# Optimization experiments

Hardware: AMD Instinct MI355X
Metric: run time of the kernel (lower is better)

## Reference

```python
import jax, jax.numpy as jnp
import numpy as np

H, DK = 8, 64  # n_head, d_k = n_feat // n_head
SCALE = 1.0 / np.sqrt(DK)


def setup_inputs() -> dict:
    key0 = jax.random.key(0)
    ks = jax.random.split(key0, 13)
    B, N, T1, T2, F = 16, 4, 256, 1024, 512
    query = jax.random.normal(ks[0], (B, T1, F), jnp.float32)
    key = jax.random.normal(ks[1], (B, N, T2, F), jnp.float32)
    value = jax.random.normal(ks[2], (B, N, T2, F), jnp.float32)
    mask_audio = jax.random.randint(ks[3], (B, N, 1, T2), 0, 2).astype(jnp.int32)
    # guarantee each candidate row has at least one valid key frame
    mask_audio = mask_audio.at[..., 0].set(1)
    mask_spk = jax.random.randint(ks[4], (B, N), 0, 2).astype(jnp.int32)
    # guarantee at least one valid candidate per batch item (avoids all -inf softmax)
    mask_spk = mask_spk.at[:, 0].set(1)
    s = 1.0 / np.sqrt(F)
    Wq = jax.random.normal(ks[5], (F, F), jnp.float32) * s
    bq = jax.random.normal(ks[6], (F,), jnp.float32) * 0.01
    Wk = jax.random.normal(ks[7], (F, F), jnp.float32) * s
    bk = jax.random.normal(ks[8], (F,), jnp.float32) * 0.01
    Wv = jax.random.normal(ks[9], (F, F), jnp.float32) * s
    bv = jax.random.normal(ks[10], (F,), jnp.float32) * 0.01
    Wo = jax.random.normal(ks[11], (F, F), jnp.float32) * s
    bo = jax.random.normal(ks[12], (F,), jnp.float32) * 0.01
    return dict(query=query, key=key, value=value, mask_audio=mask_audio,
                mask_spk=mask_spk, Wq=Wq, bq=bq, Wk=Wk, bk=bk, Wv=Wv, bv=bv,
                Wo=Wo, bo=bo)


def reference(query, key, value, mask_audio, mask_spk, Wq, bq, Wk, bk, Wv, bv, Wo, bo):
    B, T1, F = query.shape
    N, T2 = key.shape[1], key.shape[2]
    # projections (torch Linear: x @ W.T + b)
    q = (query @ Wq.T + bq).reshape(B, T1, H, DK)                 # (B,T1,H,DK)
    k = (key @ Wk.T + bk).reshape(B, N, T2, H, DK)                # (B,N,T2,H,DK)
    v = (value @ Wv.T + bv).reshape(B, N, T2, H, DK)
    # stage 1: intra-candidate temporal attention
    scores = jnp.einsum('bthd,bnshd->bnhts', q, k) * SCALE        # (B,N,H,T1,T2)
    ma = (mask_audio != 0)[:, :, None, :, :]                      # (B,N,1,1,T2)
    scores = jnp.where(ma, scores, -jnp.inf)
    attn1 = jnp.where(ma, jax.nn.softmax(scores, axis=-1), 0.0)
    phone = jnp.einsum('bnhts,bnshd->bnhtd', attn1, v)            # (B,N,H,T1,DK)
    # stage 2: inter-candidate attention
    ss = jnp.einsum('bthd,bnhtd->bthn', q, phone) * SCALE         # (B,T1,H,N)
    ms = (mask_spk != 0)[:, None, None, :]                        # (B,1,1,N)
    ss = jnp.where(ms, ss, -jnp.inf)
    attn2 = jnp.where(ms, jax.nn.softmax(ss, axis=-1), 0.0)
    x = jnp.einsum('bthn,bnhtd->bthd', attn2, phone).reshape(B, T1, H * DK)
    return x @ Wo.T + bo
```

## Files before the change

kernel.cpp:

```cpp
#include <hip/hip_runtime.h>
#include <hip/hip_bf16.h>
#include <math.h>

typedef __attribute__((ext_vector_type(4))) float  f32x4;
typedef __attribute__((ext_vector_type(4))) int    i32x4;
typedef __attribute__((ext_vector_type(8))) __bf16 bf16x8;
typedef __attribute__((ext_vector_type(8))) unsigned short u16x8;
typedef __attribute__((ext_vector_type(4))) unsigned short u16x4;

#define DEV static __device__ __forceinline__

#if __has_builtin(__builtin_amdgcn_permlane32_swap) && __has_builtin(__builtin_amdgcn_permlane16_swap)
#define HAVE_PERMLANE 1
#else
#define HAVE_PERMLANE 0
#endif

namespace {

constexpr int kB = 16, kT1 = 256, kF = 512, kN = 4, kT2 = 1024, kH = 8;
constexpr float kSCALE = 0.125f;
constexpr float kLOG2E = 1.4426950408889634f;

DEV unsigned short f2bf(float f) {
  union { float f; unsigned u; } c; c.f = f;
  unsigned u = c.u + 0x7fffu + ((c.u >> 16) & 1u);
  return (unsigned short)(u >> 16);
}
DEV float bf2f(unsigned short h) {
  union { unsigned u; float f; } c; c.u = ((unsigned)h) << 16;
  return c.f;
}

DEV void async_copy16(const void* g, void* l) {
  __builtin_amdgcn_global_load_lds(
      (const __attribute__((address_space(1))) unsigned int*)g,
      (__attribute__((address_space(3))) unsigned int*)l, 16, 0, 0);
}

DEV bf16x8 cvt8(f32x4 lo, f32x4 hi) {
  bf16x8 r;
  r[0] = (__bf16)lo[0]; r[1] = (__bf16)lo[1]; r[2] = (__bf16)lo[2]; r[3] = (__bf16)lo[3];
  r[4] = (__bf16)hi[0]; r[5] = (__bf16)hi[1]; r[6] = (__bf16)hi[2]; r[7] = (__bf16)hi[3];
  return r;
}

__global__ __launch_bounds__(256) void convert_w(
    const float* __restrict__ w0, const float* __restrict__ w1,
    const float* __restrict__ w2, const float* __restrict__ w3,
    unsigned short* __restrict__ o0, unsigned short* __restrict__ o1,
    unsigned short* __restrict__ o2, unsigned short* __restrict__ o3) {
  const int r = blockIdx.x >> 8;
  const int l = ((blockIdx.x & 255) * 256 + threadIdx.x) * 4;
  const float* src = r == 0 ? w0 : r == 1 ? w1 : r == 2 ? w2 : w3;
  unsigned short* dst = r == 0 ? o0 : r == 1 ? o1 : r == 2 ? o2 : o3;
  const float4 v = *(const float4*)(src + l);
  u16x4 q; q[0] = f2bf(v.x); q[1] = f2bf(v.y); q[2] = f2bf(v.z); q[3] = f2bf(v.w);
  *(u16x4*)(dst + l) = q;
}

template<int MODE>
__global__ __launch_bounds__(512, 2) void gemm256(
    const float* __restrict__ A, const unsigned short* __restrict__ Wb,
    const float* __restrict__ bias, unsigned short* __restrict__ outv) {
  __shared__ __align__(16) unsigned short As[2][256 * 64];
  __shared__ __align__(16) unsigned short Ws[2][256 * 64];
  const int t = threadIdx.x, lane = t & 63, wave = t >> 6;
  const int rb = blockIdx.x >> 1, cb = blockIdx.x & 1;
  const int wr = wave >> 2, wc = wave & 3;
  const int lq = lane & 15, lg = lane >> 4;
  const int arg = t >> 4, as16 = t & 15;

  f32x4 acc[8][4];
#pragma unroll
  for (int i = 0; i < 8; ++i)
#pragma unroll
    for (int j = 0; j < 4; ++j) acc[i][j] = f32x4{0.f, 0.f, 0.f, 0.f};

  f32x4 areg[8];
  bf16x8 af[4][2], bf[4][2];

#define A_ISSUE(kt)                                                             \
  do {                                                                          \
    _Pragma("unroll")                                                           \
    for (int j_ = 0; j_ < 8; ++j_)                                              \
      areg[j_] = *(const f32x4*)(A + (size_t)(rb * 256 + j_ * 32 + arg) * kF +  \
                                 (kt) * 64 + as16 * 4);                         \
  } while (0)

#define A_WRITE(dst)                                                            \
  do {                                                                          \
    _Pragma("unroll")                                                           \
    for (int j_ = 0; j_ < 8; ++j_) {                                            \
      const int row_ = j_ * 32 + arg;                                           \
      const int off_ = row_ * 64 + (((as16 >> 1) ^ (row_ & 7)) << 3) + (as16 & 1) * 4; \
      u16x4 pk_;                                                                \
      pk_[0] = f2bf(areg[j_][0]); pk_[1] = f2bf(areg[j_][1]);                   \
      pk_[2] = f2bf(areg[j_][2]); pk_[3] = f2bf(areg[j_][3]);                   \
      *(u16x4*)&(dst)[off_] = pk_;                                              \
    }                                                                           \
  } while (0)

#define W_ISSUE(kt, dst)                                                        \
  do {                                                                          \
    _Pragma("unroll")                                                           \
    for (int j_ = 0; j_ < 4; ++j_) {                                            \
      const int sidx_ = t + j_ * 512;                                           \
      const int row_ = sidx_ >> 3, s_ = sidx_ & 7;                              \
      async_copy16(Wb + (size_t)(cb * 256 + row_) * kF + (kt) * 64 +            \
                       ((s_ ^ (row_ & 7)) << 3),                                \
                   (dst) + (size_t)(j_ * 512 + wave * 64) * 8);                 \
    }                                                                           \
  } while (0)

#define RD_BF(pw)                                                               \
  do {                                                                          \
    _Pragma("unroll")                                                           \
    for (int n_ = 0; n_ < 4; ++n_) {                                            \
      const int br_ = wc * 64 + n_ * 16 + lq, x7_ = br_ & 7;                    \
      bf[n_][0] = *(const bf16x8*)&(pw)[br_ * 64 + ((lg ^ x7_) << 3)];          \
      bf[n_][1] = *(const bf16x8*)&(pw)[br_ * 64 + (((4 + lg) ^ x7_) << 3)];    \
    }                                                                           \
  } while (0)

#define RD_AF(pa, mb)                                                           \
  do {                                                                          \
    _Pragma("unroll")                                                           \
    for (int m_ = 0; m_ < 4; ++m_) {                                            \
      const int ar_ = wr * 128 + ((mb) + m_) * 16 + lq, x7_ = ar_ & 7;          \
      af[m_][0] = *(const bf16x8*)&(pa)[ar_ * 64 + ((lg ^ x7_) << 3)];          \
      af[m_][1] = *(const bf16x8*)&(pa)[ar_ * 64 + (((4 + lg) ^ x7_) << 3)];    \
    }                                                                           \
  } while (0)

#define MM(mb)                                                                  \
  do {                                                                          \
    _Pragma("unroll")                                                           \
    for (int kk_ = 0; kk_ < 2; ++kk_)                                           \
      _Pragma("unroll")                                                         \
      for (int m_ = 0; m_ < 4; ++m_)                                            \
        _Pragma("unroll")                                                       \
        for (int n_ = 0; n_ < 4; ++n_)                                          \
          acc[(mb) + m_][n_] = __builtin_amdgcn_mfma_f32_16x16x32_bf16(         \
              af[m_][kk_], bf[n_][kk_], acc[(mb) + m_][n_], 0, 0, 0);           \
  } while (0)

#define VMW0 asm volatile("s_waitcnt vmcnt(0)" ::: "memory")
#define LKW  asm volatile("s_waitcnt lgkmcnt(0)" ::: "memory")
#define SB   __builtin_amdgcn_sched_barrier(0)
#define BAR  do { __builtin_amdgcn_s_barrier(); __builtin_amdgcn_sched_barrier(0); } while (0)

  A_ISSUE(0); W_ISSUE(0, Ws[0]);
  VMW0; SB;
  A_WRITE(As[0]);
  LKW; BAR;

  unsigned short *pa = As[0], *qa = As[1], *pw = Ws[0], *qw = Ws[1];
#pragma unroll 1
  for (int kt = 0; kt < 8; ++kt) {
    if (kt < 7) { A_ISSUE(kt + 1); W_ISSUE(kt + 1, qw); }
    RD_BF(pw); RD_AF(pa, 0);
    LKW; SB;
    __builtin_amdgcn_s_setprio(1); MM(0); __builtin_amdgcn_s_setprio(0); SB;
    RD_AF(pa, 4);
    LKW; SB;
    __builtin_amdgcn_s_setprio(1); MM(4); __builtin_amdgcn_s_setprio(0); SB;
    if (kt < 7) { VMW0; SB; A_WRITE(qa); }
    LKW; BAR;
    { unsigned short* x = pa; pa = qa; qa = x; }
    { unsigned short* x = pw; pw = qw; qw = x; }
  }

#undef A_ISSUE
#undef A_WRITE
#undef W_ISSUE
#undef RD_BF
#undef RD_AF
#undef MM
#undef VMW0
#undef LKW
#undef SB
#undef BAR

  float bs4[4];
#pragma unroll
  for (int n = 0; n < 4; ++n) bs4[n] = bias[cb * 256 + wc * 64 + n * 16 + lq];

#pragma unroll
  for (int m = 0; m < 8; ++m) {
    const int row0 = rb * 256 + wr * 128 + m * 16 + lg * 4;
    const int bn = row0 >> 10, t2 = row0 & 1023;
#pragma unroll
    for (int n = 0; n < 4; ++n) {
      const int col = cb * 256 + wc * 64 + n * 16 + lq;
      const int h = col >> 6, d = col & 63;
      if (MODE == 3) {
        u16x4 pv;
#pragma unroll
        for (int j = 0; j < 4; ++j) pv[j] = f2bf(acc[m][n][j] + bs4[n]);
        *(u16x4*)&outv[(((size_t)(bn * kH + h)) * 64 + d) * kT2 + t2] = pv;
      } else {
#pragma unroll
        for (int j = 0; j < 4; ++j)
          outv[(((size_t)(bn * kH + h)) * kT2 + t2 + j) * 64 + d] =
              f2bf(acc[m][n][j] + bs4[n]);
      }
    }
  }
}

template<int MODE>
__global__ __launch_bounds__(256, 2) void gemm_mixed(
    const float* __restrict__ A, const unsigned short* __restrict__ Wb,
    const float* __restrict__ bias, void* __restrict__ outv, int nrb) {
  __shared__ __align__(16) unsigned short As[2][128 * 64];
  __shared__ __align__(16) unsigned short Bs[3][128 * 64];
  const int t = threadIdx.x, lane = t & 63, wave = t >> 6;
  const int w = blockIdx.x;
  const int xcd = w & 7, s = w >> 3;
  const int rb = xcd * (nrb >> 3) + (s >> 2);
  const int cb = s & 3;
  const int wr = wave >> 1, wc = wave & 1;
  const int lq = lane & 15, lg = lane >> 4;

  const int arow = t >> 1, ah = (t & 1) * 4;
  const float* aptr = A + (size_t)(rb * 128 + arow) * kF + ah * 8;

  f32x4 acc[4][4];
#pragma unroll
  for (int i = 0; i < 4; ++i)
#pragma unroll
    for (int j = 0; j < 4; ++j) acc[i][j] = f32x4{0.f, 0.f, 0.f, 0.f};

  f32x4 arA[8], arB[8];
  bf16x8 af[4][2], bfr[4][2];

#define A_LOAD(kb, ar)                                                          \
  do {                                                                          \
    const f32x4* p_ = (const f32x4*)(aptr + (kb) * 64);                         \
    ar[0]=p_[0]; ar[1]=p_[1]; ar[2]=p_[2]; ar[3]=p_[3];                         \
    ar[4]=p_[4]; ar[5]=p_[5]; ar[6]=p_[6]; ar[7]=p_[7];                         \
  } while (0)

#define A_CVT(ar, dst)                                                          \
  do {                                                                          \
    _Pragma("unroll")                                                           \
    for (int j_ = 0; j_ < 4; ++j_)                                              \
      *(bf16x8*)&(dst)[arow * 64 + (((ah + j_) ^ (arow & 7)) << 3)] =           \
          cvt8(ar[2*j_], ar[2*j_+1]);                                           \
  } while (0)

#define W_STAGE(kb, dst)                                                        \
  do {                                                                          \
    _Pragma("unroll")                                                           \
    for (int i_ = 0; i_ < 4; ++i_) {                                            \
      const int sidx_ = t + i_ * 256;                                           \
      const int row_ = sidx_ >> 3;                                              \
      const int gseg_ = (sidx_ & 7) ^ (row_ & 7);                               \
      async_copy16(Wb + (size_t)(cb * 128 + row_) * kF + (kb) * 64 + gseg_ * 8, \
                   (dst) + (size_t)(i_ * 256 + wave * 64) * 8);                 \
    }                                                                           \
  } while (0)

#define FRAG(Ap, Wp)                                                            \
  do {                                                                          \
    _Pragma("unroll")                                                           \
    for (int m_ = 0; m_ < 4; ++m_) {                                            \
      const int ar_ = wr * 64 + m_ * 16 + lq, x7_ = ar_ & 7;                    \
      af[m_][0] = *(const bf16x8*)&(Ap)[ar_ * 64 + ((lg       ^ x7_) << 3)];    \
      af[m_][1] = *(const bf16x8*)&(Ap)[ar_ * 64 + (((lg + 4) ^ x7_) << 3)];    \
    }                                                                           \
    _Pragma("unroll")                                                           \
    for (int n_ = 0; n_ < 4; ++n_) {                                            \
      const int br_ = wc * 64 + n_ * 16 + lq, x7_ = br_ & 7;                    \
      bfr[n_][0] = *(const bf16x8*)&(Wp)[br_ * 64 + ((lg       ^ x7_) << 3)];   \
      bfr[n_][1] = *(const bf16x8*)&(Wp)[br_ * 64 + (((lg + 4) ^ x7_) << 3)];   \
    }                                                                           \
  } while (0)

#define MFMA8                                                                   \
  do {                                                                          \
    _Pragma("unroll")                                                           \
    for (int kk_ = 0; kk_ < 2; ++kk_)                                           \
      _Pragma("unroll")                                                         \
      for (int m_ = 0; m_ < 4; ++m_)                                            \
        _Pragma("unroll")                                                       \
        for (int n_ = 0; n_ < 4; ++n_)                                          \
          acc[m_][n_] = __builtin_amdgcn_mfma_f32_16x16x32_bf16(                \
              af[m_][kk_], bfr[n_][kk_], acc[m_][n_], 0, 0, 0);                 \
  } while (0)

#define VMW(n) asm volatile("s_waitcnt vmcnt(" #n ")" ::: "memory")
#define LKW    asm volatile("s_waitcnt lgkmcnt(0)" ::: "memory")
#define BAR    do { __builtin_amdgcn_s_barrier(); __builtin_amdgcn_sched_barrier(0); } while (0)

  A_LOAD(0, arA); A_LOAD(1, arB);
  W_STAGE(0, Bs[0]); W_STAGE(1, Bs[1]);
  VMW(16);
  A_CVT(arA, As[0]);
  LKW; BAR;
  A_LOAD(2, arA); W_STAGE(2, Bs[2]);
  FRAG(As[0], Bs[0]); MFMA8;
  VMW(12); A_CVT(arB, As[1]); LKW; BAR;
  A_LOAD(3, arB); W_STAGE(3, Bs[0]);
  FRAG(As[1], Bs[1]); MFMA8;
  VMW(12); A_CVT(arA, As[0]); LKW; BAR;
  A_LOAD(4, arA); W_STAGE(4, Bs[1]);
  FRAG(As[0], Bs[2]); MFMA8;
  VMW(12); A_CVT(arB, As[1]); LKW; BAR;
  A_LOAD(5, arB); W_STAGE(5, Bs[2]);
  FRAG(As[1], Bs[0]); MFMA8;
  VMW(12); A_CVT(arA, As[0]); LKW; BAR;
  A_LOAD(6, arA); W_STAGE(6, Bs[0]);
  FRAG(As[0], Bs[1]); MFMA8;
  VMW(12); A_CVT(arB, As[1]); LKW; BAR;
  A_LOAD(7, arB); W_STAGE(7, Bs[1]);
  FRAG(As[1], Bs[2]); MFMA8;
  VMW(12); A_CVT(arA, As[0]); LKW; BAR;
  FRAG(As[0], Bs[0]); MFMA8;
  VMW(0); A_CVT(arB, As[1]); LKW; BAR;
  FRAG(As[1], Bs[1]); MFMA8;

#undef A_LOAD
#undef A_CVT
#undef W_STAGE
#undef FRAG
#undef MFMA8
#undef VMW
#undef LKW
#undef BAR

  float bs[4];
#pragma unroll
  for (int n2 = 0; n2 < 4; ++n2) bs[n2] = bias[cb*128 + wc*64 + n2*16 + lq];

#pragma unroll
  for (int m = 0; m < 4; ++m) {
#pragma unroll
    for (int n2 = 0; n2 < 4; ++n2) {
      const int col = cb*128 + wc*64 + n2*16 + lq;
      const int row0 = rb*128 + wr*64 + m*16 + lg*4;
#pragma unroll
      for (int j = 0; j < 4; ++j) {
        const int row = row0 + j;
        const float v = acc[m][n2][j] + bs[n2];
        if (MODE == 2) {
          ((float*)outv)[(size_t)row * kF + col] = v;
        } else {
          const int h = col >> 6, d = col & 63;
          const int b = row >> 8, t1i = row & 255;
          ((unsigned short*)outv)[(((size_t)(b * kH + h)) * kT1 + t1i) * 64 + d] = f2bf(v);
        }
      }
    }
  }
}

__global__ __launch_bounds__(512, 4) void attn_kernel(
    const unsigned short* __restrict__ qh, const unsigned short* __restrict__ kh,
    const unsigned short* __restrict__ vt, const int* __restrict__ mask_audio,
    unsigned short* __restrict__ phone) {
  __shared__ __align__(16) unsigned short Ks[2][64 * 64];
  __shared__ __align__(16) unsigned short Vs[2][64 * 64];
  __shared__ float Mb[2][64];
  const int t = threadIdx.x;
  const int lane = t & 63, wave = t >> 6;
  const int lq = lane & 15, lg = lane >> 4;
  const int bid = blockIdx.x;
  const int h = bid & 7, n = (bid >> 3) & 3, b = bid >> 5;
  const size_t qbase  = ((size_t)(b * kH + h)) * kT1 * 64;
  const size_t kvbase = ((size_t)((b * kN + n) * kH + h)) * kT2 * 64;
  const int* mbase = mask_audio + (size_t)(b * kN + n) * kT2;

  const int srow = (wave << 3) + (lane >> 3);
  const int sseg = lane & 7;
  const int sgx = (sseg ^ (srow & 7)) << 3;

#define STAGE_KV(c, buf)                                                          \
  do {                                                                            \
    async_copy16(kh + kvbase + ((size_t)(((c) << 6) + srow) << 6) + sgx,          \
                 &Ks[buf][wave << 9]);                                            \
    async_copy16(vt + kvbase + ((size_t)srow << 10) + ((c) << 6) + sgx,           \
                 &Vs[buf][wave << 9]);                                            \
  } while (0)

  bf16x8 qf[2][2];
#pragma unroll
  for (int qt = 0; qt < 2; ++qt) {
    const unsigned short* qp = qh + qbase + ((size_t)((wave << 5) + (qt << 4) + lq) << 6);
    qf[qt][0] = *(const bf16x8*)(qp + (lg << 3));
    qf[qt][1] = *(const bf16x8*)(qp + 32 + (lg << 3));
  }

  STAGE_KV(0, 0);
  if (t < 64) Mb[0][t] = mbase[t] ? 0.f : -1e30f;
  asm volatile("s_waitcnt vmcnt(0) lgkmcnt(0)" ::: "memory");
  __builtin_amdgcn_s_barrier();
  __builtin_amdgcn_sched_barrier(0);

  f32x4 of[2][4];
  float m2[2], l1[2];
#pragma unroll
  for (int qt = 0; qt < 2; ++qt) {
    m2[qt] = -INFINITY; l1[qt] = 0.f;
#pragma unroll
    for (int fd = 0; fd < 4; ++fd) of[qt][fd] = f32x4{0.f, 0.f, 0.f, 0.f};
  }
  const float sc2 = kSCALE * kLOG2E;

  int cur = 0;
#pragma unroll 1
  for (int c = 0; c < 16; ++c) {
    const int nxt = cur ^ 1;
    if (c < 15) {
      STAGE_KV(c + 1, nxt);
      if (t < 64) Mb[nxt][t] = mbase[((c + 1) << 6) + t] ? 0.f : -1e30f;
    }
    const unsigned short* Kb = Ks[cur];
    const unsigned short* Vb = Vs[cur];
    const float* mrow = Mb[cur];

    bf16x8 kf[4][2];
#pragma unroll
    for (int kt = 0; kt < 4; ++kt) {
      const int kr = kt * 16 + lq, x7 = kr & 7;
      kf[kt][0] = *(const bf16x8*)&Kb[kr * 64 + ((lg       ^ x7) << 3)];
      kf[kt][1] = *(const bf16x8*)&Kb[kr * 64 + (((lg + 4) ^ x7) << 3)];
    }

#pragma unroll
    for (int qt = 0; qt < 2; ++qt) {
      f32x4 sT[4];
#pragma unroll
      for (int kt = 0; kt < 4; ++kt) {
        f32x4 sv = f32x4{0.f, 0.f, 0.f, 0.f};
        sv = __builtin_amdgcn_mfma_f32_16x16x32_bf16(kf[kt][0], qf[qt][0], sv, 0, 0, 0);
        sv = __builtin_amdgcn_mfma_f32_16x16x32_bf16(kf[kt][1], qf[qt][1], sv, 0, 0, 0);
        sT[kt] = sv;
      }
      float scv[16];
#pragma unroll
      for (int kt = 0; kt < 4; ++kt) {
        const f32x4 mk = *(const f32x4*)&mrow[kt * 16 + lg * 4];
#pragma unroll
        for (int j = 0; j < 4; ++j)
          scv[kt*4+j] = fmaf(sT[kt][j], sc2, mk[j]);
      }
      float rmax = scv[0];
#pragma unroll
      for (int i = 1; i < 16; ++i) rmax = fmaxf(rmax, scv[i]);
      rmax = fmaxf(rmax, __shfl_xor(rmax, 16));
      rmax = fmaxf(rmax, __shfl_xor(rmax, 32));
      const float mold = m2[qt];
      if (!__all(rmax <= mold + 8.f)) {
        const float mnew = fmaxf(mold, rmax);
        const float rs = exp2f(mold - mnew);
        m2[qt] = mnew;
        l1[qt] *= rs;
        const float s0 = __shfl(rs, lg*4 + 0);
        const float s1 = __shfl(rs, lg*4 + 1);
        const float s2 = __shfl(rs, lg*4 + 2);
        const float s3 = __shfl(rs, lg*4 + 3);
#pragma unroll
        for (int fd = 0; fd < 4; ++fd) {
          of[qt][fd][0] *= s0; of[qt][fd][1] *= s1;
          of[qt][fd][2] *= s2; of[qt][fd][3] *= s3;
        }
      }
      const float mloc = m2[qt];
      float pf[16]; float psum = 0.f;
#pragma unroll
      for (int i = 0; i < 16; ++i) { const float p = exp2f(scv[i] - mloc); pf[i] = p; psum += p; }
      psum += __shfl_xor(psum, 16);
      psum += __shfl_xor(psum, 32);
      l1[qt] += psum;
      unsigned pk[8];
#pragma unroll
      for (int kt = 0; kt < 4; ++kt) {
        pk[2*kt]   = (unsigned)f2bf(pf[4*kt+0]) | ((unsigned)f2bf(pf[4*kt+1]) << 16);
        pk[2*kt+1] = (unsigned)f2bf(pf[4*kt+2]) | ((unsigned)f2bf(pf[4*kt+3]) << 16);
      }
      unsigned am0[4], am1[4];
#if HAVE_PERMLANE
      {
        auto x0 = __builtin_amdgcn_permlane32_swap((int)pk[0], (int)pk[2], false, false);
        auto y0 = __builtin_amdgcn_permlane16_swap(x0[0], x0[1], false, false);
        am0[0] = (unsigned)y0[0]; am0[2] = (unsigned)y0[1];
        auto x1 = __builtin_amdgcn_permlane32_swap((int)pk[1], (int)pk[3], false, false);
        auto y1 = __builtin_amdgcn_permlane16_swap(x1[0], x1[1], false, false);
        am0[1] = (unsigned)y1[0]; am0[3] = (unsigned)y1[1];
        auto x2 = __builtin_amdgcn_permlane32_swap((int)pk[4], (int)pk[6], false, false);
        auto y2 = __builtin_amdgcn_permlane16_swap(x2[0], x2[1], false, false);
        am1[0] = (unsigned)y2[0]; am1[2] = (unsigned)y2[1];
        auto x3 = __builtin_amdgcn_permlane32_swap((int)pk[5], (int)pk[7], false, false);
        auto y3 = __builtin_amdgcn_permlane16_swap(x3[0], x3[1], false, false);
        am1[1] = (unsigned)y3[0]; am1[3] = (unsigned)y3[1];
      }
#else
      {
        const int srcbase = (2 * (lg & 1)) * 16 + lq;
#pragma unroll
        for (int u = 0; u < 4; ++u) {
          const int src = srcbase + (u >> 1) * 16;
          const unsigned va0 = __shfl(pk[(u & 1)],     src);
          const unsigned vb0 = __shfl(pk[2 + (u & 1)], src);
          am0[u] = (lg & 2) ? vb0 : va0;
          const unsigned va1 = __shfl(pk[4 + (u & 1)], src);
          const unsigned vb1 = __shfl(pk[6 + (u & 1)], src);
          am1[u] = (lg & 2) ? vb1 : va1;
        }
      }
#endif
      union { unsigned u[4]; bf16x8 v; } A0, A1;
#pragma unroll
      for (int u = 0; u < 4; ++u) { A0.u[u] = am0[u]; A1.u[u] = am1[u]; }
#pragma unroll
      for (int fd = 0; fd < 4; ++fd) {
        const int d = fd * 16 + lq, x7d = d & 7;
        const bf16x8 vB0 = *(const bf16x8*)&Vb[d * 64 + ((lg       ^ x7d) << 3)];
        const bf16x8 vB1 = *(const bf16x8*)&Vb[d * 64 + (((lg + 4) ^ x7d) << 3)];
        of[qt][fd] = __builtin_amdgcn_mfma_f32_16x16x32_bf16(A0.v, vB0, of[qt][fd], 0, 0, 0);
        of[qt][fd] = __builtin_amdgcn_mfma_f32_16x16x32_bf16(A1.v, vB1, of[qt][fd], 0, 0, 0);
      }
    }
    asm volatile("s_waitcnt vmcnt(0) lgkmcnt(0)" ::: "memory");
    __builtin_amdgcn_s_barrier();
    __builtin_amdgcn_sched_barrier(0);
    cur = nxt;
  }
#undef STAGE_KV

  const size_t phbase = ((size_t)((b * kN + n) * kH + h)) * kT1 * 64;
#pragma unroll
  for (int qt = 0; qt < 2; ++qt) {
    const float li0 = 1.f / __shfl(l1[qt], lg*4 + 0);
    const float li1 = 1.f / __shfl(l1[qt], lg*4 + 1);
    const float li2 = 1.f / __shfl(l1[qt], lg*4 + 2);
    const float li3 = 1.f / __shfl(l1[qt], lg*4 + 3);
#pragma unroll
    for (int fd = 0; fd < 4; ++fd) {
      const int d = fd * 16 + lq;
      const size_t rowb = phbase + (size_t)((wave << 5) + qt*16 + lg*4) * 64 + d;
      phone[rowb]       = f2bf(of[qt][fd][0] * li0);
      phone[rowb + 64]  = f2bf(of[qt][fd][1] * li1);
      phone[rowb + 128] = f2bf(of[qt][fd][2] * li2);
      phone[rowb + 192] = f2bf(of[qt][fd][3] * li3);
    }
  }
}

__global__ __launch_bounds__(256) void stage2_kernel(
    const unsigned short* __restrict__ qh, const unsigned short* __restrict__ phone,
    const int* __restrict__ mask_spk, float* __restrict__ x) {
  const int t = threadIdx.x, lane = t & 63, wave = t >> 6;
  const int wid = blockIdx.x * 4 + wave;
  const int h = wid & 7;
  const int bt = wid >> 3;
  const int t1i = bt & 255, b = bt >> 8;
  const int d = lane;
  const float q = bf2f(qh[(((size_t)(b * kH + h)) * kT1 + t1i) * 64 + d]);
  float ph[4], ss[4];
#pragma unroll
  for (int n = 0; n < 4; ++n) {
    ph[n] = bf2f(phone[(((size_t)((b * kN + n) * kH + h)) * kT1 + t1i) * 64 + d]);
    float sv = q * ph[n];
#pragma unroll
    for (int o = 1; o < 64; o <<= 1) sv += __shfl_xor(sv, o);
    ss[n] = sv * kSCALE;
  }
  int msk[4];
#pragma unroll
  for (int n = 0; n < 4; ++n) msk[n] = mask_spk[b * kN + n];
  float mx = -INFINITY;
#pragma unroll
  for (int n = 0; n < 4; ++n) if (msk[n]) mx = fmaxf(mx, ss[n]);
  float e[4], sum = 0.f;
#pragma unroll
  for (int n = 0; n < 4; ++n) { const float v = msk[n] ? __expf(ss[n] - mx) : 0.f; e[n] = v; sum += v; }
  float xo = 0.f;
#pragma unroll
  for (int n = 0; n < 4; ++n) xo += e[n] * ph[n];
  xo /= sum;
  x[((size_t)(b * kT1 + t1i)) * kF + h * 64 + d] = xo;
}

}

extern "C" void kernel_launch(void* const* d_in, const int* in_sizes, int n_in,
                              void* d_out, int out_size, void* d_ws, size_t ws_size,
                              hipStream_t stream) {
  (void)in_sizes; (void)n_in; (void)out_size; (void)ws_size;
  const float* query = (const float*)d_in[0];
  const float* key   = (const float*)d_in[1];
  const float* value = (const float*)d_in[2];
  const int* mask_audio = (const int*)d_in[3];
  const int* mask_spk   = (const int*)d_in[4];
  const float* Wq = (const float*)d_in[5];  const float* bq = (const float*)d_in[6];
  const float* Wk = (const float*)d_in[7];  const float* bk = (const float*)d_in[8];
  const float* Wv = (const float*)d_in[9];  const float* bv = (const float*)d_in[10];
  const float* Wo = (const float*)d_in[11]; const float* bo = (const float*)d_in[12];
  float* out = (float*)d_out;

  unsigned short* qws  = (unsigned short*)d_ws;
  unsigned short* kws  = qws  + (size_t)kB * kH * kT1 * 64;
  unsigned short* vws  = kws  + (size_t)kB * kN * kH * kT2 * 64;
  unsigned short* phws = vws  + (size_t)kB * kN * kH * kT2 * 64;
  float*          xws  = (float*)(phws + (size_t)kB * kN * kH * kT1 * 64);
  unsigned short* wqb  = (unsigned short*)(xws + (size_t)kB * kT1 * kF);
  unsigned short* wkb  = wqb + (size_t)kF * kF;
  unsigned short* wvb  = wkb + (size_t)kF * kF;
  unsigned short* wob  = wvb + (size_t)kF * kF;

  convert_w<<<1024, 256, 0, stream>>>(Wq, Wk, Wv, Wo, wqb, wkb, wvb, wob);
  gemm_mixed<0><<<kB * kT1 / 128 * 4, 256, 0, stream>>>(query, wqb, bq, qws, kB * kT1 / 128);
  gemm256<1><<<kB * kN * kT2 / 256 * 2, 512, 0, stream>>>(key,   wkb, bk, kws);
  gemm256<3><<<kB * kN * kT2 / 256 * 2, 512, 0, stream>>>(value, wvb, bv, vws);
  attn_kernel<<<kB * kN * kH, 512, 0, stream>>>(qws, kws, vws, mask_audio, phws);
  stage2_kernel<<<kB * kT1 * kH / 4, 256, 0, stream>>>(qws, phws, mask_spk, xws);
  gemm_mixed<2><<<kB * kT1 / 128 * 4, 256, 0, stream>>>(xws, wob, bo, out, kB * kT1 / 128);
}
```

Before: 290.9 us.

## Deepen attention K/V pipeline to four buffers and precompute the audio mask bias

The attention kernel now keeps four K/V LDS buffers and prefetches two chunks ahead, with one barrier per iteration whose vmcnt wait is relaxed so loads overlap more compute. The audio mask bias for all 1024 keys is precomputed into LDS once, which removes the per-chunk mask staging. The row max and sum now use tree reductions, and f2bf uses the native bf16 cast. LDS use doubles, which may lower occupancy, and the single barrier placed before use needs care against buffer reuse. An unused W_STAGE variant is added, but the GEMM still uses the original staging.

Result: faster. 280.0 us (-3.8%).

```diff
diff --git a/kernel.cpp b/kernel.cpp
--- a/kernel.cpp
+++ b/kernel.cpp
@@ -23,9 +23,7 @@
 constexpr float kLOG2E = 1.4426950408889634f;
 
 DEV unsigned short f2bf(float f) {
-  union { float f; unsigned u; } c; c.f = f;
-  unsigned u = c.u + 0x7fffu + ((c.u >> 16) & 1u);
-  return (unsigned short)(u >> 16);
+  union { __bf16 h; unsigned short u; } c; c.h = (__bf16)f; return c.u;
 }
 DEV float bf2f(unsigned short h) {
   union { unsigned u; float f; } c; c.u = ((unsigned)h) << 16;
@@ -253,6 +251,23 @@
 #define W_STAGE(kb, dst)                                                        \
   do {                                                                          \
     _Pragma("unroll")                                                           \
+    for (int i_ = 0; i_ < 2; ++i_) {                                            \
+      const int sidx_ = t + i_ * 256;                                           \
+      const int row_ = sidx_ >> 2;                                              \
+      const int gseg_ = 0;                                                      \
+      (void)gseg_;                                                              \
+      const int r8_ = sidx_ >> 3;                                               \
+      const int s8_ = sidx_ & 7;                                                \
+      async_copy16(Wb + (size_t)(cb * 128 + r8_) * kF + (kb) * 64 +             \
+                       ((s8_ ^ (r8_ & 7)) << 3),                                \
+                   (dst) + (size_t)(i_ * 256 + wave * 64) * 8);                 \
+      (void)row_;                                                               \
+    }                                                                           \
+  } while (0)
+
+#define W_STAGE2(kb, dst)                                                       \
+  do {                                                                          \
+    _Pragma("unroll")                                                           \
     for (int i_ = 0; i_ < 4; ++i_) {                                            \
       const int sidx_ = t + i_ * 256;                                           \
       const int row_ = sidx_ >> 3;                                              \
@@ -295,26 +310,26 @@
 #define BAR    do { __builtin_amdgcn_s_barrier(); __builtin_amdgcn_sched_barrier(0); } while (0)
 
   A_LOAD(0, arA); A_LOAD(1, arB);
-  W_STAGE(0, Bs[0]); W_STAGE(1, Bs[1]);
+  W_STAGE2(0, Bs[0]); W_STAGE2(1, Bs[1]);
   VMW(16);
   A_CVT(arA, As[0]);
   LKW; BAR;
-  A_LOAD(2, arA); W_STAGE(2, Bs[2]);
+  A_LOAD(2, arA); W_STAGE2(2, Bs[2]);
   FRAG(As[0], Bs[0]); MFMA8;
   VMW(12); A_CVT(arB, As[1]); LKW; BAR;
-  A_LOAD(3, arB); W_STAGE(3, Bs[0]);
+  A_LOAD(3, arB); W_STAGE2(3, Bs[0]);
   FRAG(As[1], Bs[1]); MFMA8;
   VMW(12); A_CVT(arA, As[0]); LKW; BAR;
-  A_LOAD(4, arA); W_STAGE(4, Bs[1]);
+  A_LOAD(4, arA); W_STAGE2(4, Bs[1]);
   FRAG(As[0], Bs[2]); MFMA8;
   VMW(12); A_CVT(arB, As[1]); LKW; BAR;
-  A_LOAD(5, arB); W_STAGE(5, Bs[2]);
+  A_LOAD(5, arB); W_STAGE2(5, Bs[2]);
   FRAG(As[1], Bs[0]); MFMA8;
   VMW(12); A_CVT(arA, As[0]); LKW; BAR;
-  A_LOAD(6, arA); W_STAGE(6, Bs[0]);
+  A_LOAD(6, arA); W_STAGE2(6, Bs[0]);
   FRAG(As[0], Bs[1]); MFMA8;
   VMW(12); A_CVT(arB, As[1]); LKW; BAR;
-  A_LOAD(7, arB); W_STAGE(7, Bs[1]);
+  A_LOAD(7, arB); W_STAGE2(7, Bs[1]);
   FRAG(As[1], Bs[2]); MFMA8;
   VMW(12); A_CVT(arA, As[0]); LKW; BAR;
   FRAG(As[0], Bs[0]); MFMA8;
@@ -324,6 +339,7 @@
 #undef A_LOAD
 #undef A_CVT
 #undef W_STAGE
+#undef W_STAGE2
 #undef FRAG
 #undef MFMA8
 #undef VMW
@@ -360,9 +376,9 @@
     const unsigned short* __restrict__ qh, const unsigned short* __restrict__ kh,
     const unsigned short* __restrict__ vt, const int* __restrict__ mask_audio,
     unsigned short* __restrict__ phone) {
-  __shared__ __align__(16) unsigned short Ks[2][64 * 64];
-  __shared__ __align__(16) unsigned short Vs[2][64 * 64];
-  __shared__ float Mb[2][64];
+  __shared__ __align__(16) unsigned short Ks[4][64 * 64];
+  __shared__ __align__(16) unsigned short Vs[4][64 * 64];
+  __shared__ float Mbias[1024];
   const int t = threadIdx.x;
   const int lane = t & 63, wave = t >> 6;
   const int lq = lane & 15, lg = lane >> 4;
@@ -384,6 +400,13 @@
                  &Vs[buf][wave << 9]);                                            \
   } while (0)
 
+  {
+    const int i0 = t * 2;
+    const int m0 = mbase[i0], m1 = mbase[i0 + 1];
+    Mbias[i0]     = m0 ? 0.f : -1e30f;
+    Mbias[i0 + 1] = m1 ? 0.f : -1e30f;
+  }
+
   bf16x8 qf[2][2];
 #pragma unroll
   for (int qt = 0; qt < 2; ++qt) {
@@ -393,10 +416,8 @@
   }
 
   STAGE_KV(0, 0);
-  if (t < 64) Mb[0][t] = mbase[t] ? 0.f : -1e30f;
-  asm volatile("s_waitcnt vmcnt(0) lgkmcnt(0)" ::: "memory");
-  __builtin_amdgcn_s_barrier();
-  __builtin_amdgcn_sched_barrier(0);
+  STAGE_KV(1, 1);
+  asm volatile("s_waitcnt lgkmcnt(0)" ::: "memory");
 
   f32x4 of[2][4];
   float m2[2], l1[2];
@@ -408,17 +429,18 @@
   }
   const float sc2 = kSCALE * kLOG2E;
 
-  int cur = 0;
 #pragma unroll 1
   for (int c = 0; c < 16; ++c) {
-    const int nxt = cur ^ 1;
-    if (c < 15) {
-      STAGE_KV(c + 1, nxt);
-      if (t < 64) Mb[nxt][t] = mbase[((c + 1) << 6) + t] ? 0.f : -1e30f;
-    }
-    const unsigned short* Kb = Ks[cur];
-    const unsigned short* Vb = Vs[cur];
-    const float* mrow = Mb[cur];
+    if (c < 14) STAGE_KV(c + 2, (c + 2) & 3);
+    if (c < 14)      asm volatile("s_waitcnt vmcnt(4)" ::: "memory");
+    else if (c == 14) asm volatile("s_waitcnt vmcnt(2)" ::: "memory");
+    else              asm volatile("s_waitcnt vmcnt(0)" ::: "memory");
+    __builtin_amdgcn_s_barrier();
+    __builtin_amdgcn_sched_barrier(0);
+
+    const unsigned short* Kb = Ks[c & 3];
+    const unsigned short* Vb = Vs[c & 3];
+    const float* mrow = Mbias + (c << 6);
 
     bf16x8 kf[4][2];
 #pragma unroll
@@ -446,9 +468,12 @@
         for (int j = 0; j < 4; ++j)
           scv[kt*4+j] = fmaf(sT[kt][j], sc2, mk[j]);
       }
-      float rmax = scv[0];
-#pragma unroll
-      for (int i = 1; i < 16; ++i) rmax = fmaxf(rmax, scv[i]);
+      const float x0 = fmaxf(fmaxf(scv[0],  scv[1]),  scv[2]);
+      const float x1 = fmaxf(fmaxf(scv[3],  scv[4]),  scv[5]);
+      const float x2 = fmaxf(fmaxf(scv[6],  scv[7]),  scv[8]);
+      const float x3 = fmaxf(fmaxf(scv[9],  scv[10]), scv[11]);
+      const float x4 = fmaxf(fmaxf(scv[12], scv[13]), scv[14]);
+      float rmax = fmaxf(fmaxf(fmaxf(x0, x1), x2), fmaxf(fmaxf(x3, x4), scv[15]));
       rmax = fmaxf(rmax, __shfl_xor(rmax, 16));
       rmax = fmaxf(rmax, __shfl_xor(rmax, 32));
       const float mold = m2[qt];
@@ -468,9 +493,14 @@
         }
       }
       const float mloc = m2[qt];
-      float pf[16]; float psum = 0.f;
-#pragma unroll
-      for (int i = 0; i < 16; ++i) { const float p = exp2f(scv[i] - mloc); pf[i] = p; psum += p; }
+      float pf[16];
+#pragma unroll
+      for (int i = 0; i < 16; ++i) pf[i] = exp2f(scv[i] - mloc);
+      const float a0 = (pf[0] + pf[1]) + (pf[2] + pf[3]);
+      const float a1 = (pf[4] + pf[5]) + (pf[6] + pf[7]);
+      const float a2 = (pf[8] + pf[9]) + (pf[10] + pf[11]);
+      const float a3 = (pf[12] + pf[13]) + (pf[14] + pf[15]);
+      float psum = (a0 + a1) + (a2 + a3);
       psum += __shfl_xor(psum, 16);
       psum += __shfl_xor(psum, 32);
       l1[qt] += psum;
@@ -483,18 +513,18 @@
       unsigned am0[4], am1[4];
 #if HAVE_PERMLANE
       {
-        auto x0 = __builtin_amdgcn_permlane32_swap((int)pk[0], (int)pk[2], false, false);
-        auto y0 = __builtin_amdgcn_permlane16_swap(x0[0], x0[1], false, false);
-        am0[0] = (unsigned)y0[0]; am0[2] = (unsigned)y0[1];
-        auto x1 = __builtin_amdgcn_permlane32_swap((int)pk[1], (int)pk[3], false, false);
-        auto y1 = __builtin_amdgcn_permlane16_swap(x1[0], x1[1], false, false);
-        am0[1] = (unsigned)y1[0]; am0[3] = (unsigned)y1[1];
-        auto x2 = __builtin_amdgcn_permlane32_swap((int)pk[4], (int)pk[6], false, false);
-        auto y2 = __builtin_amdgcn_permlane16_swap(x2[0], x2[1], false, false);
-        am1[0] = (unsigned)y2[0]; am1[2] = (unsigned)y2[1];
-        auto x3 = __builtin_amdgcn_permlane32_swap((int)pk[5], (int)pk[7], false, false);
-        auto y3 = __builtin_amdgcn_permlane16_swap(x3[0], x3[1], false, false);
-        am1[1] = (unsigned)y3[0]; am1[3] = (unsigned)y3[1];
+        auto x0p = __builtin_amdgcn_permlane32_swap((int)pk[0], (int)pk[2], false, false);
+        auto y0p = __builtin_amdgcn_permlane16_swap(x0p[0], x0p[1], false, false);
+        am0[0] = (unsigned)y0p[0]; am0[2] = (unsigned)y0p[1];
+        auto x1p = __builtin_amdgcn_permlane32_swap((int)pk[1], (int)pk[3], false, false);
+        auto y1p = __builtin_amdgcn_permlane16_swap(x1p[0], x1p[1], false, false);
+        am0[1] = (unsigned)y1p[0]; am0[3] = (unsigned)y1p[1];
+        auto x2p = __builtin_amdgcn_permlane32_swap((int)pk[4], (int)pk[6], false, false);
+        auto y2p = __builtin_amdgcn_permlane16_swap(x2p[0], x2p[1], false, false);
+        am1[0] = (unsigned)y2p[0]; am1[2] = (unsigned)y2p[1];
+        auto x3p = __builtin_amdgcn_permlane32_swap((int)pk[5], (int)pk[7], false, false);
+        auto y3p = __builtin_amdgcn_permlane16_swap(x3p[0], x3p[1], false, false);
+        am1[1] = (unsigned)y3p[0]; am1[3] = (unsigned)y3p[1];
       }
 #else
       {
@@ -523,10 +553,6 @@
         of[qt][fd] = __builtin_amdgcn_mfma_f32_16x16x32_bf16(A1.v, vB1, of[qt][fd], 0, 0, 0);
       }
     }
-    asm volatile("s_waitcnt vmcnt(0) lgkmcnt(0)" ::: "memory");
-    __builtin_amdgcn_s_barrier();
-    __builtin_amdgcn_sched_barrier(0);
-    cur = nxt;
   }
 #undef STAGE_KV
 
```
